# Optimization experiments

Measured on AMD Instinct MI355X. Metric: run time of the kernel, lower is better.

The kernel has to match this reference:

```python
import jax, jax.numpy as jnp
import numpy as np

N, S, D = 4, 2048, 1024
H, HD = 16, 64  # heads, head_dim = patch_size // heads
SCALE = 1.0 / np.float32(np.sqrt(D))  # module divides by sqrt(patch_size), not sqrt(head_dim)


def setup_inputs() -> dict:
    key = jax.random.key(0)
    ks = jax.random.split(key, 8)
    return {
        "values": jax.random.normal(ks[0], (N, S, D), dtype=jnp.float32),
        "keys": jax.random.normal(ks[1], (N, S, D), dtype=jnp.float32),
        "query": jax.random.normal(ks[2], (N, S, D), dtype=jnp.float32),
        "Wv": jax.random.normal(ks[3], (HD, HD), dtype=jnp.float32) / np.float32(np.sqrt(HD)),
        "Wk": jax.random.normal(ks[4], (HD, HD), dtype=jnp.float32) / np.float32(np.sqrt(HD)),
        "Wq": jax.random.normal(ks[5], (HD, HD), dtype=jnp.float32) / np.float32(np.sqrt(HD)),
        "Wo": jax.random.normal(ks[6], (D, D), dtype=jnp.float32) / np.float32(np.sqrt(D)),
        "bo": jnp.zeros((D,), dtype=jnp.float32),
    }


def reference(values, keys, query, Wv, Wk, Wq, Wo, bo):
    n, ql = query.shape[0], query.shape[1]
    # reshape to heads, then per-head shared linear projections (torch Linear: x @ W.T)
    v = jnp.einsum('nlhd,ed->nlhe', values.reshape(n, -1, H, HD), Wv)
    k = jnp.einsum('nkhd,ed->nkhe', keys.reshape(n, -1, H, HD), Wk)
    q = jnp.einsum('nqhd,ed->nqhe', query.reshape(n, -1, H, HD), Wq)
    energy = jnp.einsum('nqhd,nkhd->nhqk', q, k)  # [N,H,Sq,Sk]
    attn = jax.nn.softmax(energy * SCALE, axis=3)
    out = jnp.einsum('nhql,nlhd->nqhd', attn, v).reshape(n, ql, H * HD)
    return out @ Wo.T + bo
```

## Files before the change

kernel.cpp:

```cpp
#include <hip/hip_runtime.h>
#include <stdint.h>

typedef _Float16 f16;
typedef f16 half2_t __attribute__((ext_vector_type(2)));
typedef f16 half4_t __attribute__((ext_vector_type(4)));
typedef f16 half8_t __attribute__((ext_vector_type(8)));
typedef __fp16 fp16x2_t __attribute__((ext_vector_type(2)));
typedef float f32x4 __attribute__((ext_vector_type(4)));

#define N_ 4
#define S_ 2048
#define D_ 1024
#define H_ 16
#define HD_ 64
#define LOG2E 1.44269504088896340736f
#define SCALE_ 0.03125f

typedef __attribute__((address_space(1))) void gvoid;
typedef __attribute__((address_space(3))) void lvoid;

__device__ __forceinline__ void load_lds16(const void* g, void* l) {
  __builtin_amdgcn_global_load_lds((gvoid*)(uintptr_t)g, (lvoid*)l, 16, 0, 0);
}

__device__ __forceinline__ f32x4 mfma32(half8_t a, half8_t b, f32x4 c) {
  return __builtin_amdgcn_mfma_f32_16x16x32_f16(a, b, c, 0, 0, 0);
}

__device__ __forceinline__ half2_t pack_f16(float a, float b) {
  fp16x2_t t = __builtin_amdgcn_cvt_pkrtz(a, b);
  return __builtin_bit_cast(half2_t, t);
}

__global__ void wprep(const float* __restrict__ Wv, const float* __restrict__ Wo,
                      const float* __restrict__ Wq, const float* __restrict__ Wk,
                      f16* __restrict__ Wbig, float* __restrict__ Mq) {
  int b = blockIdx.x;
  if (b < 1024) {
    int j = b;
#pragma unroll
    for (int c = 0; c < 4; ++c) {
      int i = c * 256 + threadIdx.x;
      int h = i >> 6, dd = i & 63;
      const float* wo = Wo + (size_t)j * 1024 + h * 64;
      float acc = 0.f;
#pragma unroll 8
      for (int e = 0; e < 64; ++e) acc += Wv[e * 64 + dd] * wo[e];
      Wbig[(size_t)j * 1024 + i] = (f16)acc;
    }
  } else {
    int tid = (b - 1024) * 256 + threadIdx.x;
    int d = tid >> 6, e = tid & 63;
    float acc = 0.f;
#pragma unroll 8
    for (int r = 0; r < 64; ++r) acc += Wq[r * 64 + d] * Wk[r * 64 + e];
    Mq[d * 64 + e] = acc * (SCALE_ * LOG2E);
  }
}

__global__ __launch_bounds__(256) void prep2(const float* __restrict__ Q,
                                             const float* __restrict__ K,
                                             const float* __restrict__ V,
                                             const float* __restrict__ Mq,
                                             f16* __restrict__ q16, f16* __restrict__ k16,
                                             f16* __restrict__ v16) {
  __shared__ char smem[16384];
  int b = blockIdx.x;
  if (b < 512) {
    float* mql = (float*)smem;
#pragma unroll
    for (int c = 0; c < 16; ++c) mql[c * 256 + threadIdx.x] = Mq[c * 256 + threadIdx.x];
    __syncthreads();
    int n = b >> 7, sblk = b & 127;
    int L = threadIdx.x & 63, w = threadIdx.x >> 6;
    int lq = L & 15, hh = w * 4 + (L >> 4);
    int s = sblk * 16 + lq;
    const float* qrow = Q + ((size_t)(n * S_ + s)) * D_ + hh * HD_;
    f32x4 acc4[16];
#pragma unroll
    for (int i = 0; i < 16; ++i) acc4[i] = (f32x4){0.f, 0.f, 0.f, 0.f};
    for (int d4 = 0; d4 < 16; ++d4) {
      f32x4 qv = *(const f32x4*)(qrow + d4 * 4);
#pragma unroll
      for (int dj = 0; dj < 4; ++dj) {
        const f32x4* mrow = (const f32x4*)(mql + (d4 * 4 + dj) * 64);
        float qs = qv[dj];
#pragma unroll
        for (int i = 0; i < 16; ++i) acc4[i] += mrow[i] * qs;
      }
    }
    size_t cbase = ((size_t)((n * 16 + hh) * 128 + sblk)) * 2;
#pragma unroll
    for (int dp = 0; dp < 2; ++dp) {
#pragma unroll
      for (int qd = 0; qd < 4; ++qd) {
        half8_t hv;
        f32x4 a0 = acc4[dp * 8 + qd * 2], a1 = acc4[dp * 8 + qd * 2 + 1];
#pragma unroll
        for (int j = 0; j < 4; ++j) { hv[j] = (f16)a0[j]; hv[4 + j] = (f16)a1[j]; }
        *(half8_t*)(q16 + (cbase + dp) * 512 + (qd * 16 + lq) * 8) = hv;
      }
    }
    const float* krow = K + ((size_t)(n * S_ + s)) * D_ + hh * HD_;
    f32x4 kr[16];
#pragma unroll
    for (int i = 0; i < 16; ++i) kr[i] = *(const f32x4*)(krow + i * 4);
#pragma unroll
    for (int dp = 0; dp < 2; ++dp) {
#pragma unroll
      for (int qd = 0; qd < 4; ++qd) {
        half8_t hv;
        f32x4 a0 = kr[dp * 8 + qd * 2], a1 = kr[dp * 8 + qd * 2 + 1];
#pragma unroll
        for (int j = 0; j < 4; ++j) { hv[j] = (f16)a0[j]; hv[4 + j] = (f16)a1[j]; }
        *(half8_t*)(k16 + (cbase + dp) * 512 + (qd * 16 + lq) * 8) = hv;
      }
    }
  } else {
    f16* lv = (f16*)smem;
    int b2 = b - 512;
    int n = b2 >> 10, hh = (b2 >> 6) & 15, sb = b2 & 63;
    int t = threadIdx.x;
    {
      int r = t >> 3, ic = t & 7;
      const float* src = V + ((size_t)(n * S_ + sb * 32 + r)) * D_ + hh * HD_ + ic * 8;
      f32x4 a = *(const f32x4*)src;
      f32x4 b3 = *(const f32x4*)(src + 4);
      half8_t hv;
#pragma unroll
      for (int j = 0; j < 4; ++j) { hv[j] = (f16)a[j]; hv[4 + j] = (f16)b3[j]; }
      *(half8_t*)(lv + r * 64 + ic * 8) = hv;
    }
    __syncthreads();
    {
      int mt = t >> 6, L = t & 63;
      int quad = L >> 4, ld = L & 15;
      half8_t o;
#pragma unroll
      for (int j = 0; j < 4; ++j) {
        o[j]     = lv[(quad * 4 + j) * 64 + mt * 16 + ld];
        o[4 + j] = lv[(quad * 4 + j + 16) * 64 + mt * 16 + ld];
      }
      *(half8_t*)(v16 + (((size_t)(n * 16 + hh) * 64 + sb) * 4 + mt) * 512 + L * 8) = o;
    }
  }
}

__global__ __launch_bounds__(256, 2) void flash(const f16* __restrict__ q16,
                                                const f16* __restrict__ k16,
                                                const f16* __restrict__ v16,
                                                f16* __restrict__ att) {
  __shared__ char lds[32768];
  int nh = blockIdx.x;
  int qt = blockIdx.y;
  int L = threadIdx.x & 63, w = threadIdx.x >> 6;
  int lq = L & 15, quad = L >> 4;

  const half8_t* qg = (const half8_t*)q16;
  half8_t qB[4][2];
#pragma unroll
  for (int j = 0; j < 4; ++j) {
    size_t qc = ((size_t)(nh * 128 + qt * 16 + w * 4 + j)) * 2;
    qB[j][0] = qg[qc * 64 + L];
    qB[j][1] = qg[(qc + 1) * 64 + L];
  }

  f32x4 accO[4][4];
#pragma unroll
  for (int j = 0; j < 4; ++j)
#pragma unroll
    for (int i = 0; i < 4; ++i) accO[j][i] = (f32x4){0.f, 0.f, 0.f, 0.f};
  f32x4 lvec[4];
#pragma unroll
  for (int j = 0; j < 4; ++j) lvec[j] = (f32x4){0.f, 0.f, 0.f, 0.f};

  const char* kg = (const char*)k16 + (size_t)nh * 262144 + w * 2048 + L * 16;
  const char* vg = (const char*)v16 + (size_t)nh * 262144 + w * 2048 + L * 16;

#pragma unroll
  for (int t = 0; t < 2; ++t)
#pragma unroll
    for (int c = 0; c < 2; ++c) {
      load_lds16(kg + t * 8192 + c * 1024, lds + t * 8192 + w * 2048 + c * 1024);
      load_lds16(vg + t * 8192 + c * 1024, lds + 16384 + t * 8192 + w * 2048 + c * 1024);
    }
  __syncthreads();

  for (int it = 0; it < 32; ++it) {
    const char* kb = lds + (it & 1) * 8192;
    const char* vb = lds + 16384 + (it & 1) * 8192;
#pragma unroll
    for (int g = 0; g < 2; ++g) {
      half4_t pcg[4][2];
#pragma unroll
      for (int u = 0; u < 2; ++u) {
        int mt = 2 * g + u;
        half8_t k0 = *(const half8_t*)(kb + (mt * 2 + 0) * 1024 + L * 16);
        half8_t k1 = *(const half8_t*)(kb + (mt * 2 + 1) * 1024 + L * 16);
#pragma unroll
        for (int j = 0; j < 4; ++j) {
          f32x4 a = (f32x4){0.f, 0.f, 0.f, 0.f};
          __builtin_amdgcn_s_setprio(1);
          a = mfma32(k0, qB[j][0], a);
          a = mfma32(k1, qB[j][1], a);
          __builtin_amdgcn_s_setprio(0);
          f32x4 p;
#pragma unroll
          for (int r = 0; r < 4; ++r) p[r] = __builtin_amdgcn_exp2f(a[r]);
          lvec[j] += p;
          half2_t c01 = pack_f16(p[0], p[1]);
          half2_t c23 = pack_f16(p[2], p[3]);
          pcg[j][u] = __builtin_shufflevector(c01, c23, 0, 1, 2, 3);
        }
      }
      half8_t pb[4];
#pragma unroll
      for (int j = 0; j < 4; ++j)
        pb[j] = __builtin_shufflevector(pcg[j][0], pcg[j][1], 0, 1, 2, 3, 4, 5, 6, 7);
      __builtin_amdgcn_s_setprio(1);
#pragma unroll
      for (int mt2 = 0; mt2 < 4; ++mt2) {
        half8_t vf = *(const half8_t*)(vb + (g * 4 + mt2) * 1024 + L * 16);
#pragma unroll
        for (int j = 0; j < 4; ++j)
          accO[j][mt2] = mfma32(vf, pb[j], accO[j][mt2]);
      }
      __builtin_amdgcn_s_setprio(0);
    }
    __syncthreads();
    if (it + 2 < 32) {
      char* dk = lds + (it & 1) * 8192 + w * 2048;
      char* dv = lds + 16384 + (it & 1) * 8192 + w * 2048;
#pragma unroll
      for (int c = 0; c < 2; ++c) {
        load_lds16(kg + (size_t)(it + 2) * 8192 + c * 1024, dk + c * 1024);
        load_lds16(vg + (size_t)(it + 2) * 8192 + c * 1024, dv + c * 1024);
      }
    }
  }

  int n = nh >> 4, h = nh & 15;
#pragma unroll
  for (int j = 0; j < 4; ++j) {
    float l = lvec[j][0] + lvec[j][1] + lvec[j][2] + lvec[j][3];
    l += __shfl_xor(l, 16, 64);
    l += __shfl_xor(l, 32, 64);
    float inv_l = 1.0f / l;
    int s = qt * 256 + w * 64 + j * 16 + lq;
    f16* orow = att + ((size_t)(n * S_ + s)) * D_ + h * HD_;
#pragma unroll
    for (int mt2 = 0; mt2 < 4; ++mt2) {
      half4_t o;
#pragma unroll
      for (int r = 0; r < 4; ++r) o[r] = (f16)(accO[j][mt2][r] * inv_l);
      *(half4_t*)(orow + mt2 * 16 + quad * 4) = o;
    }
  }
}

__global__ __launch_bounds__(256, 2) void ogemm(const f16* __restrict__ A, const f16* __restrict__ Bm,
                                                const float* __restrict__ bias, float* __restrict__ C) {
  __shared__ char lds[32768];
  int bm = blockIdx.x, bn = blockIdx.y;
  int L = threadIdx.x & 63, w = threadIdx.x >> 6;
  int wm = w >> 1, wn = w & 1;
  int lq = L & 15, quad = L >> 4;
  int lr = L >> 2, lc = L & 3;
  int src_c = lc ^ (lr & 3);
  f32x4 acc[16];
#pragma unroll
  for (int i = 0; i < 16; ++i) acc[i] = (f32x4){0.f, 0.f, 0.f, 0.f};

  const f16* ga0 = A + ((size_t)(bm * 128 + (w * 2) * 16 + lr)) * 1024 + src_c * 8;
  const f16* gb0 = Bm + ((size_t)(bn * 128 + (w * 2) * 16 + lr)) * 1024 + src_c * 8;

#pragma unroll
  for (int t = 0; t < 2; ++t)
#pragma unroll
    for (int c = 0; c < 2; ++c) {
      load_lds16(ga0 + t * 32 + (size_t)c * 16 * 1024, lds + t * 16384 + (w * 2 + c) * 1024);
      load_lds16(gb0 + t * 32 + (size_t)c * 16 * 1024, lds + t * 16384 + 8192 + (w * 2 + c) * 1024);
    }
  __syncthreads();

  for (int kt = 0; kt < 32; ++kt) {
    const char* base = lds + (kt & 1) * 16384;
    half8_t af[4], bf[4];
#pragma unroll
    for (int t = 0; t < 4; ++t) {
      int ch = quad ^ (lq & 3);
      af[t] = *(const half8_t*)(base + (wm * 64 + t * 16 + lq) * 64 + ch * 16);
      bf[t] = *(const half8_t*)(base + 8192 + (wn * 64 + t * 16 + lq) * 64 + ch * 16);
    }
#pragma unroll
    for (int mt = 0; mt < 4; ++mt)
#pragma unroll
      for (int nt = 0; nt < 4; ++nt)
        acc[mt * 4 + nt] =
            __builtin_amdgcn_mfma_f32_16x16x32_f16(af[mt], bf[nt], acc[mt * 4 + nt], 0, 0, 0);
    __syncthreads();
    if (kt + 2 < 32) {
      char* dst = lds + (kt & 1) * 16384;
#pragma unroll
      for (int c = 0; c < 2; ++c) {
        load_lds16(ga0 + (kt + 2) * 32 + (size_t)c * 16 * 1024, dst + (w * 2 + c) * 1024);
        load_lds16(gb0 + (kt + 2) * 32 + (size_t)c * 16 * 1024, dst + 8192 + (w * 2 + c) * 1024);
      }
    }
  }

#pragma unroll
  for (int nt = 0; nt < 4; ++nt) {
    int col = bn * 128 + wn * 64 + nt * 16 + lq;
    float bv = bias[col];
#pragma unroll
    for (int mt = 0; mt < 4; ++mt) {
#pragma unroll
      for (int r = 0; r < 4; ++r) {
        int row = bm * 128 + wm * 64 + mt * 16 + quad * 4 + r;
        C[(size_t)row * 1024 + col] = acc[mt * 4 + nt][r] + bv;
      }
    }
  }
}

extern "C" void kernel_launch(void* const* d_in, const int* in_sizes, int n_in,
                              void* d_out, int out_size, void* d_ws, size_t ws_size,
                              hipStream_t stream) {
  const float* V  = (const float*)d_in[0];
  const float* K  = (const float*)d_in[1];
  const float* Q  = (const float*)d_in[2];
  const float* Wv = (const float*)d_in[3];
  const float* Wk = (const float*)d_in[4];
  const float* Wq = (const float*)d_in[5];
  const float* Wo = (const float*)d_in[6];
  const float* bo = (const float*)d_in[7];
  float* out = (float*)d_out;

  char* ws = (char*)d_ws;
  float* Mq  = (float*)(ws);
  f16* Wbig  = (f16*)(ws + (1ull << 20));
  f16* q16   = (f16*)(ws + (3ull << 20));
  f16* k16   = (f16*)(ws + (19ull << 20));
  f16* v16   = (f16*)(ws + (35ull << 20));
  f16* att   = (f16*)(ws + (51ull << 20));

  wprep<<<1040, 256, 0, stream>>>(Wv, Wo, Wq, Wk, Wbig, Mq);
  prep2<<<4608, 256, 0, stream>>>(Q, K, V, Mq, q16, k16, v16);
  flash<<<dim3(64, 8), 256, 0, stream>>>(q16, k16, v16, att);
  ogemm<<<dim3(64, 8), 256, 0, stream>>>(att, Wbig, bo, out);
}
```

Measured before the change: 271.5 us.

## Load K/V tiles directly from global into registers instead of LDS double-buffer

The flash kernel no longer stages K and V tiles through a double-buffered LDS ring with global_load_lds and block barriers. Each wave now reads the full 8 KB K and V tiles for every iteration straight from global memory into registers. This removes LDS traffic and __syncthreads, but every wave reloads the same data, which quadruples global/L2 reads. There is also no explicit prefetch, so load latency is exposed unless the compiler hoists the loads.

After: 273.9 us. Within noise of the previous version (+0.9%).

```diff
diff --git a/kernel.cpp b/kernel.cpp
--- a/kernel.cpp
+++ b/kernel.cpp
@@ -150,7 +150,6 @@
                                                 const f16* __restrict__ k16,
                                                 const f16* __restrict__ v16,
                                                 f16* __restrict__ att) {
-  __shared__ char lds[32768];
   int nh = blockIdx.x;
   int qt = blockIdx.y;
   int L = threadIdx.x & 63, w = threadIdx.x >> 6;
@@ -174,29 +173,25 @@
 #pragma unroll
   for (int j = 0; j < 4; ++j) lvec[j] = (f32x4){0.f, 0.f, 0.f, 0.f};
 
-  const char* kg = (const char*)k16 + (size_t)nh * 262144 + w * 2048 + L * 16;
-  const char* vg = (const char*)v16 + (size_t)nh * 262144 + w * 2048 + L * 16;
-
-#pragma unroll
-  for (int t = 0; t < 2; ++t)
-#pragma unroll
-    for (int c = 0; c < 2; ++c) {
-      load_lds16(kg + t * 8192 + c * 1024, lds + t * 8192 + w * 2048 + c * 1024);
-      load_lds16(vg + t * 8192 + c * 1024, lds + 16384 + t * 8192 + w * 2048 + c * 1024);
-    }
-  __syncthreads();
+  const char* kg = (const char*)k16 + (size_t)nh * 262144 + L * 16;
+  const char* vg = (const char*)v16 + (size_t)nh * 262144 + L * 16;
 
   for (int it = 0; it < 32; ++it) {
-    const char* kb = lds + (it & 1) * 8192;
-    const char* vb = lds + 16384 + (it & 1) * 8192;
+    const char* kb = kg + (size_t)it * 8192;
+    const char* vb = vg + (size_t)it * 8192;
+    half8_t kf[8], vf8[8];
+#pragma unroll
+    for (int c = 0; c < 8; ++c) kf[c] = *(const half8_t*)(kb + c * 1024);
+#pragma unroll
+    for (int c = 0; c < 8; ++c) vf8[c] = *(const half8_t*)(vb + c * 1024);
 #pragma unroll
     for (int g = 0; g < 2; ++g) {
       half4_t pcg[4][2];
 #pragma unroll
       for (int u = 0; u < 2; ++u) {
         int mt = 2 * g + u;
-        half8_t k0 = *(const half8_t*)(kb + (mt * 2 + 0) * 1024 + L * 16);
-        half8_t k1 = *(const half8_t*)(kb + (mt * 2 + 1) * 1024 + L * 16);
+        half8_t k0 = kf[mt * 2 + 0];
+        half8_t k1 = kf[mt * 2 + 1];
 #pragma unroll
         for (int j = 0; j < 4; ++j) {
           f32x4 a = (f32x4){0.f, 0.f, 0.f, 0.f};
@@ -220,22 +215,12 @@
       __builtin_amdgcn_s_setprio(1);
 #pragma unroll
       for (int mt2 = 0; mt2 < 4; ++mt2) {
-        half8_t vf = *(const half8_t*)(vb + (g * 4 + mt2) * 1024 + L * 16);
+        half8_t vf = vf8[g * 4 + mt2];
 #pragma unroll
         for (int j = 0; j < 4; ++j)
           accO[j][mt2] = mfma32(vf, pb[j], accO[j][mt2]);
       }
       __builtin_amdgcn_s_setprio(0);
-    }
-    __syncthreads();
-    if (it + 2 < 32) {
-      char* dk = lds + (it & 1) * 8192 + w * 2048;
-      char* dv = lds + 16384 + (it & 1) * 8192 + w * 2048;
-#pragma unroll
-      for (int c = 0; c < 2; ++c) {
-        load_lds16(kg + (size_t)(it + 2) * 8192 + c * 1024, dk + c * 1024);
-        load_lds16(vg + (size_t)(it + 2) * 8192 + c * 1024, dv + c * 1024);
-      }
     }
   }
 
```
